# Kernel optimization log

Hardware: AMD Instinct MI355X
Metric: run time of the kernel (lower is better)

Reference implementation:

```python
import jax, jax.numpy as jnp
import numpy as np
import math

TAU_MEM = 20.0
ALPHA = math.exp(-1.0 / TAU_MEM)
BASE_THRESHOLD = 1.0


def setup_inputs() -> dict:
    key = jax.random.key(0)
    k1, k2, k3 = jax.random.split(key, 3)
    B, T, D, H = 32, 1024, 512, 512
    x = jax.random.normal(k1, (B, T, D), dtype=jnp.float32)
    # nn.Linear default init: U(-1/sqrt(D), 1/sqrt(D))
    bound = 1.0 / math.sqrt(D)
    W = jax.random.uniform(k2, (H, D), dtype=jnp.float32, minval=-bound, maxval=bound)
    b = jax.random.uniform(k3, (H,), dtype=jnp.float32, minval=-bound, maxval=bound)
    threshold_adapt = jnp.ones((H,), dtype=jnp.float32) * BASE_THRESHOLD
    return {"x": x, "W": W, "b": b, "threshold_adapt": threshold_adapt}


def reference(x, W, b, threshold_adapt):
    B, T, D = x.shape
    H = W.shape[0]
    # One batched GEMM instead of T small ones (same math as fc(x[:, t]) per step)
    xlin = jnp.einsum('btd,hd->bth', x, W) + b  # [B, T, H]
    xlin_t = jnp.transpose(xlin, (1, 0, 2))     # [T, B, H]

    def step(mem, xt):
        mem = ALPHA * mem + xt
        # torch std: unbiased (ddof=1), over hidden dim; B>1 branch
        mem_std = jnp.std(mem, axis=-1, keepdims=True, ddof=1)  # [B, 1]
        thr = threshold_adapt[None, :] + 0.1 * mem_std           # [B, H]
        spike = (mem >= thr).astype(mem.dtype)
        mem = mem * (1.0 - spike)
        return mem, spike

    mem0 = jnp.zeros((B, H), dtype=x.dtype)
    mem, spikes_t = jax.lax.scan(step, mem0, xlin_t)
    spikes = jnp.transpose(spikes_t, (1, 0, 2))  # [B, T, H]
    return spikes, mem
```

## Files before the change

kernel.cpp:

```cpp
#include <hip/hip_runtime.h>


#define ALPHA_F 0.95122942450071402f

constexpr int Bb = 32, T = 1024, D = 512, Hh = 512;
constexpr int M = Bb * T;
constexpr int NSCAN = 32;
constexpr int NBLOCKS = 256;
constexpr int NTILES = 512;

#define BM 128
#define BN 256
#define BK 16
#define LDA (BM + 4)
#define LDB (BN + 4)

template <int CTRL>
__device__ __forceinline__ float dpp_add(float v) {
  int s = __builtin_amdgcn_update_dpp(0, __builtin_bit_cast(int, v),
                                      CTRL, 0xF, 0xF, true);
  return v + __builtin_bit_cast(float, s);
}

__device__ __forceinline__ float dpp_reduce(float v) {
  v = dpp_add<0x111>(v);
  v = dpp_add<0x112>(v);
  v = dpp_add<0x114>(v);
  v = dpp_add<0x118>(v);
  v = dpp_add<0x142>(v);
  v = dpp_add<0x143>(v);
  return v;
}

__global__ void zero_ws_kernel(unsigned* ws) {
  if (threadIdx.x < 257) ws[threadIdx.x] = 0;
}

__global__ __launch_bounds__(512) void fused_kernel(
    const float* __restrict__ X,
    const float* __restrict__ W,
    const float* __restrict__ bias,
    const float* __restrict__ ta,
    float* out,
    float* memout,
    unsigned* ws)
{
  unsigned* prog = ws;
  unsigned* ticket = ws + 256;
  const int tid = threadIdx.x;

  if (blockIdx.x >= NSCAN) {
    __shared__ float As[2][BK][LDA];
    __shared__ float Bs[2][BK][LDB];
    __shared__ unsigned s_g;
    const int tm = tid >> 5;
    const int tn = tid & 31;
    const int sr = tid >> 2;
    const int sc4 = (tid & 3) << 2;

    float4 ra, rb0, rb1;

#define GLOAD(k0)                                                            \
  {                                                                          \
    ra  = *(const float4*)(X + (size_t)(rowA + sr) * D + (k0) + sc4);        \
    rb0 = *(const float4*)(W + (size_t)(rowB + sr) * D + (k0) + sc4);        \
    rb1 = *(const float4*)(W + (size_t)(rowB + 128 + sr) * D + (k0) + sc4);  \
  }

#define SWRITE(bf)                                                           \
  {                                                                          \
    As[bf][sc4 + 0][sr] = ra.x; As[bf][sc4 + 1][sr] = ra.y;                  \
    As[bf][sc4 + 2][sr] = ra.z; As[bf][sc4 + 3][sr] = ra.w;                  \
    Bs[bf][sc4 + 0][sr] = rb0.x; Bs[bf][sc4 + 1][sr] = rb0.y;                \
    Bs[bf][sc4 + 2][sr] = rb0.z; Bs[bf][sc4 + 3][sr] = rb0.w;                \
    Bs[bf][sc4 + 0][sr + 128] = rb1.x; Bs[bf][sc4 + 1][sr + 128] = rb1.y;    \
    Bs[bf][sc4 + 2][sr + 128] = rb1.z; Bs[bf][sc4 + 3][sr + 128] = rb1.w;    \
  }

    for (;;) {
      __syncthreads();
      if (tid == 0)
        s_g = __hip_atomic_fetch_add(ticket, 1u, __ATOMIC_RELAXED,
                                     __HIP_MEMORY_SCOPE_AGENT);
      __syncthreads();
      const unsigned g = s_g;
      if (g >= NTILES) break;
      const int chg = (int)(g >> 6);
      const int idx = (int)(g & 63u);
      const int mt  = (idx >> 1) * 8 + chg;
      const int bn  = idx & 1;
      const int rowA = mt * BM;
      const int rowB = bn * BN;

      float acc[8][8];
#pragma unroll
      for (int i = 0; i < 8; ++i)
#pragma unroll
        for (int j = 0; j < 8; ++j) acc[i][j] = 0.f;

      GLOAD(0)
      int cur = 0;
      for (int k0 = 0; k0 < D; k0 += BK) {
        SWRITE(cur)
        __syncthreads();
        if (k0 + BK < D) GLOAD(k0 + BK)
#pragma unroll
        for (int k = 0; k < BK; ++k) {
          float4 a0 = *(const float4*)&As[cur][k][tm * 4];
          float4 a1 = *(const float4*)&As[cur][k][64 + tm * 4];
          float4 b0 = *(const float4*)&Bs[cur][k][tn * 4];
          float4 b1 = *(const float4*)&Bs[cur][k][128 + tn * 4];
          float av[8] = {a0.x, a0.y, a0.z, a0.w, a1.x, a1.y, a1.z, a1.w};
          float bv[8] = {b0.x, b0.y, b0.z, b0.w, b1.x, b1.y, b1.z, b1.w};
#pragma unroll
          for (int i = 0; i < 8; ++i)
#pragma unroll
            for (int j = 0; j < 8; ++j)
              acc[i][j] = fmaf(av[i], bv[j], acc[i][j]);
        }
        cur ^= 1;
      }

      const int c0 = rowB + tn * 4;
      const int c1 = rowB + 128 + tn * 4;
      float4 bb0 = *(const float4*)(bias + c0);
      float4 bb1 = *(const float4*)(bias + c1);
      float bc[8] = {bb0.x, bb0.y, bb0.z, bb0.w, bb1.x, bb1.y, bb1.z, bb1.w};
#pragma unroll
      for (int i = 0; i < 8; ++i) {
        const int r = rowA + ((i < 4) ? (tm * 4 + i) : (64 + tm * 4 + (i - 4)));
        float4 v0, v1;
        v0.x = acc[i][0] + bc[0]; v0.y = acc[i][1] + bc[1];
        v0.z = acc[i][2] + bc[2]; v0.w = acc[i][3] + bc[3];
        v1.x = acc[i][4] + bc[4]; v1.y = acc[i][5] + bc[5];
        v1.z = acc[i][6] + bc[6]; v1.w = acc[i][7] + bc[7];
        *(float4*)(out + (size_t)r * Hh + c0) = v0;
        *(float4*)(out + (size_t)r * Hh + c1) = v1;
      }
      __syncthreads();
      if (tid == 0)
        __hip_atomic_fetch_add(prog + mt, 1u, __ATOMIC_RELEASE,
                               __HIP_MEMORY_SCOPE_AGENT);
    }
#undef GLOAD
#undef SWRITE
    return;
  }

  if (tid >= 64) return;
  __builtin_amdgcn_s_setprio(3);

  const int b = blockIdx.x;
  const int lane = tid;
  float* base = out + (size_t)b * (size_t)(T * Hh);
  const int h0 = lane * 4;
  const int h1 = 256 + lane * 4;

  float4 tav0 = *(const float4*)(ta + h0);
  float4 tav1 = *(const float4*)(ta + h1);
  float tac[8] = {tav0.x, tav0.y, tav0.z, tav0.w,
                  tav1.x, tav1.y, tav1.z, tav1.w};

#define WAIT_CHUNK(idxc)                                                     \
  {                                                                          \
    unsigned* wp = prog + (idxc);                                            \
    while (__hip_atomic_load(wp, __ATOMIC_RELAXED,                           \
                             __HIP_MEMORY_SCOPE_AGENT) < 2u) {               \
      __builtin_amdgcn_s_sleep(2);                                           \
    }                                                                        \
    __builtin_amdgcn_fence(__ATOMIC_ACQUIRE, "agent");                       \
  }

  float4 pA0[8], pB0[8], pA1[8], pB1[8];
  float cc[8], mr[8];
  bool fire[8];
#pragma unroll
  for (int i = 0; i < 8; ++i) fire[i] = false;

#define LOAD1(NA, NB, u, t)                                                  \
  NA[u] = *(const float4*)(base + (size_t)(t) * Hh + h0);                    \
  NB[u] = *(const float4*)(base + (size_t)(t) * Hh + h1);

#define STEPX(CA, CB, u, t, NXA, NXB, SPEC)                                  \
  {                                                                          \
    const float xu_[8] = {CA[u].x, CA[u].y, CA[u].z, CA[u].w,                \
                          CB[u].x, CB[u].y, CB[u].z, CB[u].w};               \
    _Pragma("unroll")                                                        \
    for (int i = 0; i < 8; ++i) mr[i] = fire[i] ? xu_[i] : cc[i];            \
    float s_ = ((mr[0] + mr[1]) + (mr[2] + mr[3])) +                         \
               ((mr[4] + mr[5]) + (mr[6] + mr[7]));                          \
    float q_ = ((fmaf(mr[0], mr[0], mr[1] * mr[1])) +                        \
                (fmaf(mr[2], mr[2], mr[3] * mr[3]))) +                       \
               ((fmaf(mr[4], mr[4], mr[5] * mr[5])) +                        \
                (fmaf(mr[6], mr[6], mr[7] * mr[7])));                        \
    if (SPEC) {           \
      const float4 nxa_ = (NXA), nxb_ = (NXB);                               \
      const float xn_[8] = {nxa_.x, nxa_.y, nxa_.z, nxa_.w,                  \
                            nxb_.x, nxb_.y, nxb_.z, nxb_.w};                 \
      _Pragma("unroll")                                                      \
      for (int i = 0; i < 8; ++i) cc[i] = fmaf(ALPHA_F, mr[i], xn_[i]);      \
    }                                                                        \
    s_ = dpp_reduce(s_);                                                     \
    q_ = dpp_reduce(q_);                                                     \
    float var_ = fmaf(s_ * s_, -(1.0f / Hh), q_) * (1.0f / (Hh - 1));        \
    var_ = fmaxf(var_, 0.f);                                                 \
    float sdl_ = __builtin_amdgcn_sqrtf(var_);            \
    const float sd_ = __builtin_bit_cast(                                    \
        float,                                                               \
        __builtin_amdgcn_readlane(__builtin_bit_cast(int, sdl_), 63));       \
    float sp_[8];                                                            \
    _Pragma("unroll")                                                        \
    for (int i = 0; i < 8; ++i) {                                            \
      fire[i] = mr[i] >= fmaf(0.1f, sd_, tac[i]);                            \
      sp_[i] = fire[i] ? 1.f : 0.f;                                          \
    }                                                                        \
    *(float4*)(base + (size_t)(t) * Hh + h0) =                               \
        make_float4(sp_[0], sp_[1], sp_[2], sp_[3]);                         \
    *(float4*)(base + (size_t)(t) * Hh + h1) =                               \
        make_float4(sp_[4], sp_[5], sp_[6], sp_[7]);                         \
  }

#define GROUP(CA, CB, NA, NB, T0, PF, LASTG)                                 \
  {                                                                          \
    if (PF) {                                                                \
      LOAD1(NA, NB, 0, (T0) + 8)  LOAD1(NA, NB, 1, (T0) + 9)                 \
      LOAD1(NA, NB, 2, (T0) + 10) LOAD1(NA, NB, 3, (T0) + 11)                \
      LOAD1(NA, NB, 4, (T0) + 12) LOAD1(NA, NB, 5, (T0) + 13)                \
      LOAD1(NA, NB, 6, (T0) + 14) LOAD1(NA, NB, 7, (T0) + 15)                \
    }                                                                        \
    STEPX(CA, CB, 0, (T0) + 0, CA[1], CB[1], 1)                              \
    STEPX(CA, CB, 1, (T0) + 1, CA[2], CB[2], 1)                              \
    STEPX(CA, CB, 2, (T0) + 2, CA[3], CB[3], 1)                              \
    STEPX(CA, CB, 3, (T0) + 3, CA[4], CB[4], 1)                              \
    STEPX(CA, CB, 4, (T0) + 4, CA[5], CB[5], 1)                              \
    STEPX(CA, CB, 5, (T0) + 5, CA[6], CB[6], 1)                              \
    STEPX(CA, CB, 6, (T0) + 6, CA[7], CB[7], 1)                              \
    STEPX(CA, CB, 7, (T0) + 7, NA[0], NB[0], !(LASTG))                       \
  }

  WAIT_CHUNK(b * 8);
  LOAD1(pA0, pB0, 0, 0) LOAD1(pA0, pB0, 1, 1)
  LOAD1(pA0, pB0, 2, 2) LOAD1(pA0, pB0, 3, 3)
  LOAD1(pA0, pB0, 4, 4) LOAD1(pA0, pB0, 5, 5)
  LOAD1(pA0, pB0, 6, 6) LOAD1(pA0, pB0, 7, 7)
  cc[0] = pA0[0].x; cc[1] = pA0[0].y; cc[2] = pA0[0].z; cc[3] = pA0[0].w;
  cc[4] = pB0[0].x; cc[5] = pB0[0].y; cc[6] = pB0[0].z; cc[7] = pB0[0].w;

  for (int gp = 0; gp < 63; ++gp) {
    const int t0 = gp << 4;
    GROUP(pA0, pB0, pA1, pB1, t0, true, false)
    if ((gp & 7) == 7) WAIT_CHUNK(b * 8 + ((t0 + 16) >> 7));
    GROUP(pA1, pB1, pA0, pB0, t0 + 8, true, false)
  }
  GROUP(pA0, pB0, pA1, pB1, 1008, true, false)
  GROUP(pA1, pB1, pA0, pB0, 1016, false, true)

#undef GROUP
#undef STEPX
#undef LOAD1
#undef WAIT_CHUNK

  float mf[8];
#pragma unroll
  for (int i = 0; i < 8; ++i) mf[i] = fire[i] ? 0.f : mr[i];
  *(float4*)(memout + (size_t)b * Hh + h0) = make_float4(mf[0], mf[1], mf[2], mf[3]);
  *(float4*)(memout + (size_t)b * Hh + h1) = make_float4(mf[4], mf[5], mf[6], mf[7]);
}

__global__ __launch_bounds__(256) void gemm_kernel(
    const float* __restrict__ X, const float* __restrict__ W,
    const float* __restrict__ bias, float* __restrict__ out) {
  const int bn = blockIdx.x, bm = blockIdx.y;
  __shared__ float As[BK][BM + 4];
  __shared__ float Bs[BK][BM + 4];
  const int tid = threadIdx.x, tm = tid >> 4, tn = tid & 15;
  float acc[8][8];
#pragma unroll
  for (int i = 0; i < 8; ++i)
#pragma unroll
    for (int j = 0; j < 8; ++j) acc[i][j] = 0.f;
  const int rowA = bm * BM, rowB = bn * BM;
  for (int k0 = 0; k0 < D; k0 += BK) {
    __syncthreads();
#pragma unroll
    for (int i = 0; i < 2; ++i) {
      const int f = tid * 2 + i, r = f >> 2, c4 = (f & 3) << 2;
      float4 a = *(const float4*)(X + (size_t)(rowA + r) * D + k0 + c4);
      As[c4 + 0][r] = a.x; As[c4 + 1][r] = a.y;
      As[c4 + 2][r] = a.z; As[c4 + 3][r] = a.w;
      float4 w = *(const float4*)(W + (size_t)(rowB + r) * D + k0 + c4);
      Bs[c4 + 0][r] = w.x; Bs[c4 + 1][r] = w.y;
      Bs[c4 + 2][r] = w.z; Bs[c4 + 3][r] = w.w;
    }
    __syncthreads();
#pragma unroll
    for (int k = 0; k < BK; ++k) {
      float4 a0 = *(const float4*)&As[k][tm * 4];
      float4 a1 = *(const float4*)&As[k][64 + tm * 4];
      float4 b0 = *(const float4*)&Bs[k][tn * 4];
      float4 b1 = *(const float4*)&Bs[k][64 + tn * 4];
      float av[8] = {a0.x, a0.y, a0.z, a0.w, a1.x, a1.y, a1.z, a1.w};
      float bv[8] = {b0.x, b0.y, b0.z, b0.w, b1.x, b1.y, b1.z, b1.w};
#pragma unroll
      for (int i = 0; i < 8; ++i)
#pragma unroll
        for (int j = 0; j < 8; ++j)
          acc[i][j] = fmaf(av[i], bv[j], acc[i][j]);
    }
  }
  const int c0 = rowB + tn * 4, c1 = rowB + 64 + tn * 4;
  float4 bb0 = *(const float4*)(bias + c0);
  float4 bb1 = *(const float4*)(bias + c1);
  float bc[8] = {bb0.x, bb0.y, bb0.z, bb0.w, bb1.x, bb1.y, bb1.z, bb1.w};
#pragma unroll
  for (int i = 0; i < 8; ++i) {
    const int r = rowA + ((i < 4) ? (tm * 4 + i) : (64 + tm * 4 + (i - 4)));
    float4 v0, v1;
    v0.x = acc[i][0] + bc[0]; v0.y = acc[i][1] + bc[1];
    v0.z = acc[i][2] + bc[2]; v0.w = acc[i][3] + bc[3];
    v1.x = acc[i][4] + bc[4]; v1.y = acc[i][5] + bc[5];
    v1.z = acc[i][6] + bc[6]; v1.w = acc[i][7] + bc[7];
    *(float4*)(out + (size_t)r * Hh + c0) = v0;
    *(float4*)(out + (size_t)r * Hh + c1) = v1;
  }
}

__global__ __launch_bounds__(64) void scan_kernel(
    float* __restrict__ xs, const float* __restrict__ ta,
    float* __restrict__ memout) {
  const int b = blockIdx.x, lane = threadIdx.x;
  float* base = xs + (size_t)b * (size_t)(T * Hh);
  const int h0 = lane * 4, h1 = 256 + lane * 4;
  float4 tav0 = *(const float4*)(ta + h0);
  float4 tav1 = *(const float4*)(ta + h1);
  float tac[8] = {tav0.x, tav0.y, tav0.z, tav0.w,
                  tav1.x, tav1.y, tav1.z, tav1.w};
  float4 pa[4], pb[4];
#pragma unroll
  for (int u = 0; u < 4; ++u) {
    pa[u] = *(const float4*)(base + (size_t)u * Hh + h0);
    pb[u] = *(const float4*)(base + (size_t)u * Hh + h1);
  }
  float xc[8], cc[8], mr[8];
  bool fire[8];
  {
    const float4 a = pa[0], bq = pb[0];
    xc[0] = a.x; xc[1] = a.y; xc[2] = a.z; xc[3] = a.w;
    xc[4] = bq.x; xc[5] = bq.y; xc[6] = bq.z; xc[7] = bq.w;
  }
#pragma unroll
  for (int i = 0; i < 8; ++i) { cc[i] = xc[i]; fire[i] = false; }
#pragma unroll 4
  for (int t = 0; t < T; ++t) {
    const int u = t & 3;
    if (t + 4 < T) {
      pa[u] = *(const float4*)(base + (size_t)(t + 4) * Hh + h0);
      pb[u] = *(const float4*)(base + (size_t)(t + 4) * Hh + h1);
    }
#pragma unroll
    for (int i = 0; i < 8; ++i) mr[i] = fire[i] ? xc[i] : cc[i];
    float s = ((mr[0] + mr[1]) + (mr[2] + mr[3])) +
              ((mr[4] + mr[5]) + (mr[6] + mr[7]));
    float q = ((mr[0] * mr[0] + mr[1] * mr[1]) +
               (mr[2] * mr[2] + mr[3] * mr[3])) +
              ((mr[4] * mr[4] + mr[5] * mr[5]) +
               (mr[6] * mr[6] + mr[7] * mr[7]));
    {
      const float4 na = pa[(u + 1) & 3];
      const float4 nb = pb[(u + 1) & 3];
      xc[0] = na.x; xc[1] = na.y; xc[2] = na.z; xc[3] = na.w;
      xc[4] = nb.x; xc[5] = nb.y; xc[6] = nb.z; xc[7] = nb.w;
#pragma unroll
      for (int i = 0; i < 8; ++i) cc[i] = fmaf(ALPHA_F, mr[i], xc[i]);
    }
    s = dpp_reduce(s);
    q = dpp_reduce(q);
    float var = fmaxf((q - s * s * (1.0f / Hh)) * (1.0f / (Hh - 1)), 0.f);
    float sdl = __builtin_amdgcn_sqrtf(var);
    const float sd = __builtin_bit_cast(
        float, __builtin_amdgcn_readlane(__builtin_bit_cast(int, sdl), 63));
    float sp[8];
#pragma unroll
    for (int i = 0; i < 8; ++i) {
      fire[i] = mr[i] >= fmaf(0.1f, sd, tac[i]);
      sp[i] = fire[i] ? 1.f : 0.f;
    }
    *(float4*)(base + (size_t)t * Hh + h0) = make_float4(sp[0], sp[1], sp[2], sp[3]);
    *(float4*)(base + (size_t)t * Hh + h1) = make_float4(sp[4], sp[5], sp[6], sp[7]);
  }
  float mf[8];
#pragma unroll
  for (int i = 0; i < 8; ++i) mf[i] = fire[i] ? 0.f : mr[i];
  *(float4*)(memout + (size_t)b * Hh + h0) = make_float4(mf[0], mf[1], mf[2], mf[3]);
  *(float4*)(memout + (size_t)b * Hh + h1) = make_float4(mf[4], mf[5], mf[6], mf[7]);
}

extern "C" void kernel_launch(void* const* d_in, const int* in_sizes, int n_in,
                              void* d_out, int out_size, void* d_ws,
                              size_t ws_size, hipStream_t stream) {
  const float* x    = (const float*)d_in[0];
  const float* W    = (const float*)d_in[1];
  const float* bias = (const float*)d_in[2];
  const float* ta   = (const float*)d_in[3];

  float* out    = (float*)d_out;
  float* spikes = out;
  float* memout = out + (size_t)Bb * T * Hh;

  if (ws_size >= 257 * sizeof(unsigned)) {
    unsigned* ws = (unsigned*)d_ws;
    zero_ws_kernel<<<dim3(1), dim3(512), 0, stream>>>(ws);
    fused_kernel<<<dim3(NBLOCKS), dim3(512), 0, stream>>>(
        x, W, bias, ta, spikes, memout, ws);
  } else {
    dim3 ggrid(Hh / 128, M / BM);
    gemm_kernel<<<ggrid, dim3(256), 0, stream>>>(x, W, bias, spikes);
    scan_kernel<<<dim3(Bb), dim3(64), 0, stream>>>(spikes, ta, memout);
  }
}
```

Baseline: 300.0 us.

## Shrink GEMM tiles to 128x128 with 256-thread blocks and more persistent blocks

Reworks the fused persistent kernel's GEMM side from 128x256 tiles with 512 threads to 128x128 tiles with 256 threads. It launches 480 blocks instead of 256, reorders the tile ticket mapping, and makes each scan chunk wait for four tile signals instead of two. The aim is more concurrent GEMM blocks and finer-grained progress signalling, so the scan blocks can start each chunk sooner. In exchange each tile reuses loaded data less, and more blocks contend on the atomic ticket counter.

```diff
diff --git a/kernel.cpp b/kernel.cpp
--- a/kernel.cpp
+++ b/kernel.cpp
@@ -6,14 +6,13 @@
 constexpr int Bb = 32, T = 1024, D = 512, Hh = 512;
 constexpr int M = Bb * T;
 constexpr int NSCAN = 32;
-constexpr int NBLOCKS = 256;
-constexpr int NTILES = 512;
+constexpr int NBLOCKS = 480;
+constexpr int NTILES = (M / 128) * (Hh / 128);
+constexpr int SIG_PER_CHUNK = 4;
 
 #define BM 128
-#define BN 256
 #define BK 16
 #define LDA (BM + 4)
-#define LDB (BN + 4)
 
 template <int CTRL>
 __device__ __forceinline__ float dpp_add(float v) {
@@ -36,7 +35,7 @@
   if (threadIdx.x < 257) ws[threadIdx.x] = 0;
 }
 
-__global__ __launch_bounds__(512) void fused_kernel(
+__global__ __launch_bounds__(256) void fused_kernel(
     const float* __restrict__ X,
     const float* __restrict__ W,
     const float* __restrict__ bias,
@@ -51,30 +50,34 @@
 
   if (blockIdx.x >= NSCAN) {
     __shared__ float As[2][BK][LDA];
-    __shared__ float Bs[2][BK][LDB];
+    __shared__ float Bs[2][BK][LDA];
     __shared__ unsigned s_g;
-    const int tm = tid >> 5;
-    const int tn = tid & 31;
-    const int sr = tid >> 2;
-    const int sc4 = (tid & 3) << 2;
-
-    float4 ra, rb0, rb1;
+    const int tm = tid >> 4;
+    const int tn = tid & 15;
+    const int f0 = tid * 2, f1 = tid * 2 + 1;
+    const int r0 = f0 >> 2, c40 = (f0 & 3) << 2;
+    const int r1 = f1 >> 2, c41 = (f1 & 3) << 2;
+
+    float4 ra0, ra1, rb0, rb1;
 
 #define GLOAD(k0)                                                            \
   {                                                                          \
-    ra  = *(const float4*)(X + (size_t)(rowA + sr) * D + (k0) + sc4);        \
-    rb0 = *(const float4*)(W + (size_t)(rowB + sr) * D + (k0) + sc4);        \
-    rb1 = *(const float4*)(W + (size_t)(rowB + 128 + sr) * D + (k0) + sc4);  \
+    ra0 = *(const float4*)(X + (size_t)(rowA + r0) * D + (k0) + c40);        \
+    ra1 = *(const float4*)(X + (size_t)(rowA + r1) * D + (k0) + c41);        \
+    rb0 = *(const float4*)(W + (size_t)(rowB + r0) * D + (k0) + c40);        \
+    rb1 = *(const float4*)(W + (size_t)(rowB + r1) * D + (k0) + c41);        \
   }
 
 #define SWRITE(bf)                                                           \
   {                                                                          \
-    As[bf][sc4 + 0][sr] = ra.x; As[bf][sc4 + 1][sr] = ra.y;                  \
-    As[bf][sc4 + 2][sr] = ra.z; As[bf][sc4 + 3][sr] = ra.w;                  \
-    Bs[bf][sc4 + 0][sr] = rb0.x; Bs[bf][sc4 + 1][sr] = rb0.y;                \
-    Bs[bf][sc4 + 2][sr] = rb0.z; Bs[bf][sc4 + 3][sr] = rb0.w;                \
-    Bs[bf][sc4 + 0][sr + 128] = rb1.x; Bs[bf][sc4 + 1][sr + 128] = rb1.y;    \
-    Bs[bf][sc4 + 2][sr + 128] = rb1.z; Bs[bf][sc4 + 3][sr + 128] = rb1.w;    \
+    As[bf][c40 + 0][r0] = ra0.x; As[bf][c40 + 1][r0] = ra0.y;                \
+    As[bf][c40 + 2][r0] = ra0.z; As[bf][c40 + 3][r0] = ra0.w;                \
+    As[bf][c41 + 0][r1] = ra1.x; As[bf][c41 + 1][r1] = ra1.y;                \
+    As[bf][c41 + 2][r1] = ra1.z; As[bf][c41 + 3][r1] = ra1.w;                \
+    Bs[bf][c40 + 0][r0] = rb0.x; Bs[bf][c40 + 1][r0] = rb0.y;                \
+    Bs[bf][c40 + 2][r0] = rb0.z; Bs[bf][c40 + 3][r0] = rb0.w;                \
+    Bs[bf][c41 + 0][r1] = rb1.x; Bs[bf][c41 + 1][r1] = rb1.y;                \
+    Bs[bf][c41 + 2][r1] = rb1.z; Bs[bf][c41 + 3][r1] = rb1.w;                \
   }
 
     for (;;) {
@@ -85,12 +88,13 @@
       __syncthreads();
       const unsigned g = s_g;
       if (g >= NTILES) break;
-      const int chg = (int)(g >> 6);
-      const int idx = (int)(g & 63u);
-      const int mt  = (idx >> 1) * 8 + chg;
-      const int bn  = idx & 1;
-      const int rowA = mt * BM;
-      const int rowB = bn * BN;
+      const int ch = (int)(g >> 7);
+      const int idx = (int)(g & 127u);
+      const int b  = idx >> 2;
+      const int bn = idx & 3;
+      const int bm = b * 8 + ch;
+      const int rowA = bm * BM;
+      const int rowB = bn * BM;
 
       float acc[8][8];
 #pragma unroll
@@ -109,7 +113,7 @@
           float4 a0 = *(const float4*)&As[cur][k][tm * 4];
           float4 a1 = *(const float4*)&As[cur][k][64 + tm * 4];
           float4 b0 = *(const float4*)&Bs[cur][k][tn * 4];
-          float4 b1 = *(const float4*)&Bs[cur][k][128 + tn * 4];
+          float4 b1 = *(const float4*)&Bs[cur][k][64 + tn * 4];
           float av[8] = {a0.x, a0.y, a0.z, a0.w, a1.x, a1.y, a1.z, a1.w};
           float bv[8] = {b0.x, b0.y, b0.z, b0.w, b1.x, b1.y, b1.z, b1.w};
 #pragma unroll
@@ -122,7 +126,7 @@
       }
 
       const int c0 = rowB + tn * 4;
-      const int c1 = rowB + 128 + tn * 4;
+      const int c1 = rowB + 64 + tn * 4;
       float4 bb0 = *(const float4*)(bias + c0);
       float4 bb1 = *(const float4*)(bias + c1);
       float bc[8] = {bb0.x, bb0.y, bb0.z, bb0.w, bb1.x, bb1.y, bb1.z, bb1.w};
@@ -139,7 +143,7 @@
       }
       __syncthreads();
       if (tid == 0)
-        __hip_atomic_fetch_add(prog + mt, 1u, __ATOMIC_RELEASE,
+        __hip_atomic_fetch_add(prog + bm, 1u, __ATOMIC_RELEASE,
                                __HIP_MEMORY_SCOPE_AGENT);
     }
 #undef GLOAD
@@ -165,7 +169,8 @@
   {                                                                          \
     unsigned* wp = prog + (idxc);                                            \
     while (__hip_atomic_load(wp, __ATOMIC_RELAXED,                           \
-                             __HIP_MEMORY_SCOPE_AGENT) < 2u) {               \
+                             __HIP_MEMORY_SCOPE_AGENT) <                     \
+           (unsigned)SIG_PER_CHUNK) {                                        \
       __builtin_amdgcn_s_sleep(2);                                           \
     }                                                                        \
     __builtin_amdgcn_fence(__ATOMIC_ACQUIRE, "agent");                       \
@@ -410,7 +415,7 @@
   if (ws_size >= 257 * sizeof(unsigned)) {
     unsigned* ws = (unsigned*)d_ws;
     zero_ws_kernel<<<dim3(1), dim3(512), 0, stream>>>(ws);
-    fused_kernel<<<dim3(NBLOCKS), dim3(512), 0, stream>>>(
+    fused_kernel<<<dim3(NBLOCKS), dim3(256), 0, stream>>>(
         x, W, bias, ta, spikes, memout, ws);
   } else {
     dim3 ggrid(Hh / 128, M / BM);
```

Result: slower. 335.8 us (+11.9%).
